# Performance work log

Measured on AMD Instinct MI355X. Metric: run time of the kernel, lower is better.

The kernel has to match this reference:

```python
import jax, jax.numpy as jnp
import numpy as np

DEPTH = 6
GAMMA = 1e-4
DIM = 1024
HIDDEN = 16
OUT_DIM = 64
N = 16384


def setup_inputs() -> dict:
    key = jax.random.key(0)
    k0, k1, k2, k3, k4 = jax.random.split(key, 5)
    X = jax.random.normal(k0, (N, DIM), dtype=jnp.float32)
    s1 = 1.0 / np.sqrt(DIM)
    s2 = 1.0 / np.sqrt(HIDDEN)
    W1 = jax.random.uniform(k1, (DIM, HIDDEN), jnp.float32, -s1, s1)
    b1 = jax.random.uniform(k2, (HIDDEN,), jnp.float32, -s1, s1)
    W2 = jax.random.uniform(k3, (HIDDEN, OUT_DIM), jnp.float32, -s2, s2)
    b2 = jax.random.uniform(k4, (OUT_DIM,), jnp.float32, -s2, s2)
    return {"X": X, "W1": W1, "b1": b1, "W2": W2, "b2": b2}


def _mlp(X, W1, b1, W2, b2):
    # shared FeedForwardClassifier: Linear(dim,16) -> ReLU -> Linear(16,out_dim)
    return jax.nn.relu(X @ W1 + b1) @ W2 + b2


def reference(X, W1, b1, W2, b2):
    for _ in range(DEPTH):
        # custom LayerNorm: row-wise L2 normalization (no eps in original)
        Xn = X / jnp.linalg.norm(X, axis=-1, keepdims=True)  # [N, dim]
        P = jax.nn.softmax(_mlp(Xn, W1, b1, W2, b2), axis=-1)  # [N, out_dim]
        # X + g*P@P.T@X - g*X@X.T@X, contracted small-Gram-first (same math)
        PtX = P.T @ Xn          # [out_dim, dim]
        G = Xn.T @ Xn           # [dim, dim]
        X = Xn + GAMMA * (P @ PtX) - GAMMA * (Xn @ G)
    return _mlp(X, W1, b1, W2, b2)
```

## Files before the change

kernel.cpp:

```cpp
#include <hip/hip_runtime.h>


#define N_ROWS 16384
#define DIM 1024
#define HID 16
#define OUTD 64
#define DEPTH 6
#define GAMMA 1e-4f

typedef short bf16x8 __attribute__((ext_vector_type(8)));
typedef unsigned short u16x8 __attribute__((ext_vector_type(8)));
typedef float f32x4 __attribute__((ext_vector_type(4)));

#define AS1C(p) ((const __attribute__((address_space(1))) void*)(p))
#define AS3(p)  ((__attribute__((address_space(3))) void*)(p))

__device__ __forceinline__ unsigned short f2bf(float f) {
    unsigned u = __builtin_bit_cast(unsigned, f);
    u += 0x7fffu + ((u >> 16) & 1u);
    return (unsigned short)(u >> 16);
}
__device__ __forceinline__ float b2f(ushort u) {
    unsigned x = ((unsigned)u) << 16;
    return __builtin_bit_cast(float, x);
}
__device__ __forceinline__ int swz(int n, int row) {
    return (n & ~63) | ((((n >> 3) & 7) ^ (row & 7)) << 3) | (n & 7);
}

__device__ __forceinline__ void atom_pk_bf16(ushort* p, ushort lo, ushort hi) {
#if __has_builtin(__builtin_amdgcn_global_atomic_fadd_v2bf16)
    typedef short s16x2 __attribute__((ext_vector_type(2)));
    s16x2 v;
    v[0] = (short)lo; v[1] = (short)hi;
    __builtin_amdgcn_global_atomic_fadd_v2bf16(
        (__attribute__((address_space(1))) s16x2*)p, v);
#else
    unsigned* up = (unsigned*)p;
    unsigned expected = *up;
    while (true) {
        float flo = b2f((ushort)(expected & 0xffffu)) + b2f(lo);
        float fhi = b2f((ushort)(expected >> 16)) + b2f(hi);
        unsigned desired = (unsigned)f2bf(flo) | ((unsigned)f2bf(fhi) << 16);
        unsigned old = atomicCAS(up, expected, desired);
        if (old == expected) break;
        expected = old;
    }
#endif
}

__global__ __launch_bounds__(256) void tobf16_k(const float* __restrict__ X,
        ushort* __restrict__ Xm, float* __restrict__ rinv) {
    int row = blockIdx.x, t = threadIdx.x;
    float4 v = ((const float4*)(X + (size_t)row * DIM))[t];
    ushort4 o4;
    o4.x = f2bf(v.x); o4.y = f2bf(v.y); o4.z = f2bf(v.z); o4.w = f2bf(v.w);
    *(ushort4*)(Xm + (size_t)row * DIM + swz(t * 4, row)) = o4;
    float ss = v.x * v.x + v.y * v.y + v.z * v.z + v.w * v.w;
    for (int o = 32; o > 0; o >>= 1) ss += __shfl_down(ss, o);
    __shared__ float wsum[4];
    if ((t & 63) == 0) wsum[t >> 6] = ss;
    __syncthreads();
    if (t == 0) rinv[row] = 1.0f / sqrtf(wsum[0] + wsum[1] + wsum[2] + wsum[3]);
}

__global__ __launch_bounds__(256) void rsqrt_k(const float* __restrict__ ssacc,
        float* __restrict__ rinv) {
    int i = blockIdx.x * 256 + threadIdx.x;
    rinv[i] = 1.0f / sqrtf(ssacc[i]);
}

__global__ __launch_bounds__(256) void transpose_k(const ushort* __restrict__ Xm,
        const float* __restrict__ rinv, ushort* __restrict__ XnT) {
    int r0 = blockIdx.x * 64;
    int c0 = blockIdx.y * 64;
    int t = threadIdx.x;
    __shared__ float ts[64 * 65];
    __shared__ float riS[64];
    if (t < 64) riS[t] = rinv[r0 + t];
    __syncthreads();
#pragma unroll
    for (int i = 0; i < 2; ++i) {
        int idx = i * 256 + t;
        int r = idx >> 3, lg = idx & 7;
        int rr = r0 + r;
        const ushort* p = Xm + (size_t)rr * DIM + c0 + ((lg ^ (rr & 7)) << 3);
        u16x8 a = *(const u16x8*)p;
        float s = riS[r];
        float* d = &ts[r * 65 + lg * 8];
#pragma unroll
        for (int u = 0; u < 8; ++u) d[u] = b2f(a[u]) * s;
    }
    __syncthreads();
#pragma unroll
    for (int i = 0; i < 2; ++i) {
        int g = i * 256 + t;
        int c = g >> 3;
        int rg = g & 7;
        u16x8 pk;
#pragma unroll
        for (int u = 0; u < 8; ++u) pk[u] = f2bf(ts[(rg * 8 + u) * 65 + c]);
        *(u16x8*)(XnT + (size_t)(c0 + c) * N_ROWS + r0 + ((rg ^ (c & 7)) << 3)) = pk;
    }
}

__global__ __launch_bounds__(256) void prep_w1t_k(const float* __restrict__ W1,
        ushort* __restrict__ W1T) {
    int idx = blockIdx.x * 256 + threadIdx.x;
    int h = idx >> 10, j = idx & 1023;
    W1T[idx] = f2bf(W1[j * HID + h]);
}

__global__ __launch_bounds__(256) void zgemm_k(const ushort* __restrict__ Xm,
        const ushort* __restrict__ W1T, const float* __restrict__ b1,
        float* __restrict__ z, const float* __restrict__ rv) {
    int t = threadIdx.x;
    int wave = t >> 6, lane = t & 63;
    int rl = lane & 15, q = lane >> 4;
    int rowbase = blockIdx.x * 64 + wave * 16;
    int m = rowbase + rl;
    int msw = m & 7;
    const ushort* arow = Xm + (size_t)m * DIM;
    const ushort* brow = W1T + (size_t)rl * DIM + q * 8;
    f32x4 acc = {0.f, 0.f, 0.f, 0.f};
#pragma unroll 8
    for (int kt = 0; kt < DIM; kt += 32) {
        int gl = ((kt >> 3) & 7) | q;
        int off = (kt & ~63) + ((gl ^ msw) << 3);
        bf16x8 a = *(const bf16x8*)(arow + off);
        bf16x8 b = *(const bf16x8*)(brow + kt);
        acc = __builtin_amdgcn_mfma_f32_16x16x32_bf16(a, b, acc, 0, 0, 0);
    }
#pragma unroll
    for (int rg = 0; rg < 4; ++rg) {
        int mm = rowbase + q * 4 + rg;
        float s = rv ? rv[mm] : 1.0f;
        z[(size_t)mm * HID + rl] = acc[rg] * s + b1[rl];
    }
}

__global__ __launch_bounds__(256) void head_k(const float* __restrict__ z,
        const float* __restrict__ W2, const float* __restrict__ b2,
        ushort* __restrict__ Pb, ushort* __restrict__ PTb,
        float* __restrict__ out, int do_softmax) {
    __shared__ float w2s[HID * OUTD];
    __shared__ float b2s[OUTD];
    int t = threadIdx.x;
    ((float4*)w2s)[t] = ((const float4*)W2)[t];
    if (t < OUTD) b2s[t] = b2[t];
    __syncthreads();
    int m = blockIdx.x * 256 + t;
    float h[HID];
    const float4* zp = (const float4*)(z + (size_t)m * HID);
#pragma unroll
    for (int i = 0; i < 4; ++i) {
        float4 v = zp[i];
        h[i * 4 + 0] = fmaxf(v.x, 0.f); h[i * 4 + 1] = fmaxf(v.y, 0.f);
        h[i * 4 + 2] = fmaxf(v.z, 0.f); h[i * 4 + 3] = fmaxf(v.w, 0.f);
    }
    float lo[OUTD];
#pragma unroll
    for (int o = 0; o < OUTD; ++o) lo[o] = b2s[o];
    for (int i = 0; i < HID; ++i) {
        float hv = h[i];
#pragma unroll
        for (int o = 0; o < OUTD; ++o) lo[o] += hv * w2s[i * OUTD + o];
    }
    if (do_softmax) {
        float mx = lo[0];
#pragma unroll
        for (int o = 1; o < OUTD; ++o) mx = fmaxf(mx, lo[o]);
        float sm = 0.f;
#pragma unroll
        for (int o = 0; o < OUTD; ++o) { float e = __expf(lo[o] - mx); lo[o] = e; sm += e; }
        float inv = 1.0f / sm;
#pragma unroll
        for (int o8 = 0; o8 < 8; ++o8) {
            u16x8 pk;
#pragma unroll
            for (int u = 0; u < 8; ++u) pk[u] = f2bf(lo[o8 * 8 + u] * inv);
            ((u16x8*)(Pb + (size_t)m * OUTD))[o8 ^ (m & 7)] = pk;
        }
#pragma unroll
        for (int o = 0; o < OUTD; ++o)
            PTb[(size_t)o * N_ROWS + swz(m, o)] = f2bf(lo[o] * inv);
    } else {
        float4* op = (float4*)(out + (size_t)m * OUTD);
#pragma unroll
        for (int o4 = 0; o4 < 16; ++o4) {
            float4 v; v.x = lo[o4 * 4 + 0]; v.y = lo[o4 * 4 + 1];
            v.z = lo[o4 * 4 + 2]; v.w = lo[o4 * 4 + 3];
            op[o4] = v;
        }
    }
}

__global__ __launch_bounds__(256) void castgp_k(const ushort* __restrict__ Gacc,
        const ushort* __restrict__ PtXacc, ushort* __restrict__ Gb,
        ushort* __restrict__ PtXTb) {
    int idx = blockIdx.x * 256 + threadIdx.x;
    if (idx < 262144) {
        int n = idx >> 8;
        int so = (idx & 255) * 4;
        int k0 = (so & ~63) | ((((so >> 3) & 7) ^ (n & 7)) << 3) | (so & 7);
        ushort4 o;
        ushort v0 = (k0 + 0 > n) ? Gacc[(size_t)n * DIM + k0 + 0] : Gacc[(size_t)(k0 + 0) * DIM + n];
        ushort v1 = (k0 + 1 > n) ? Gacc[(size_t)n * DIM + k0 + 1] : Gacc[(size_t)(k0 + 1) * DIM + n];
        ushort v2 = (k0 + 2 > n) ? Gacc[(size_t)n * DIM + k0 + 2] : Gacc[(size_t)(k0 + 2) * DIM + n];
        ushort v3 = (k0 + 3 > n) ? Gacc[(size_t)n * DIM + k0 + 3] : Gacc[(size_t)(k0 + 3) * DIM + n];
        o.x = v0 ^ 0x8000u; o.y = v1 ^ 0x8000u;
        o.z = v2 ^ 0x8000u; o.w = v3 ^ 0x8000u;
        *(ushort4*)(Gb + (size_t)n * DIM + so) = o;
    } else {
        int vv = idx - 262144;
        int d = vv >> 4;
        int so = (vv & 15) * 4;
        int k0 = ((((so >> 3) & 7) ^ (d & 7)) << 3) | (so & 7);
        const ushort* src = PtXacc + (size_t)d * OUTD + k0;
        ushort4 o;
        o.x = src[0]; o.y = src[1]; o.z = src[2]; o.w = src[3];
        *(ushort4*)(PtXTb + (size_t)d * OUTD + so) = o;
    }
}

template<int BM, int BN, int EPI, int TRI>
__global__ __launch_bounds__(256, 3) void gemm_nt_k(
        const ushort* __restrict__ A0, int lda0,
        const ushort* __restrict__ B0, int ldb0, int k0len,
        const ushort* __restrict__ A1, int lda1,
        const ushort* __restrict__ B1, int ldb1, int k1len,
        float* __restrict__ C, int ldc,
        const float* __restrict__ rinv, float gamma,
        float* __restrict__ ssacc) {
    constexpr int WTN = BN / 2;
    constexpr int NF = WTN / 16;
    constexpr int NAW = BM / 64;
    constexpr int NBW = BN / 64;
    __shared__ ushort ls[(BM + BN) * 64];
    ushort* lsA = ls;
    ushort* lsB = ls + BM * 64;
    int t = threadIdx.x;
    int wave = t >> 6, lane = t & 63;
    int rl = lane & 15, q = lane >> 4;
    int wm = wave & 1, wn = wave >> 1;
    int m0, n0, zidx;
    if (TRI) {
        int bid = blockIdx.x;
        int rest = bid >> 3;
        int bx = rest % 36, tm = 0;
        int zhi = rest / 36;
        zidx = (bid & 7) | (zhi << 3);
        while (bx >= 8 - tm) { bx -= 8 - tm; ++tm; }
        m0 = tm * 128; n0 = (tm + bx) * 128;
    } else {
        m0 = blockIdx.x * BM; n0 = blockIdx.y * BN; zidx = blockIdx.z;
    }
    int lrow8 = lane >> 3, lgrp = lane & 7;
    bool isA = wave < NAW;
    bool active = wave < NAW + NBW;
    int wlocal = isA ? wave : wave - NAW;
    ushort* dstb = ls + (isA ? 0 : BM * 64) + wlocal * 4096;

    f32x4 acc[4][NF];
#pragma unroll
    for (int i = 0; i < 4; ++i)
#pragma unroll
        for (int j = 0; j < NF; ++j) acc[i][j] = f32x4{0.f, 0.f, 0.f, 0.f};
    float rvv[4][4];

    for (int seg = 0; seg < 2; ++seg) {
        int klen = seg ? k1len : k0len;
        if (klen > 0) {
            const ushort* OPA = seg ? A1 : A0;
            const ushort* OPB = seg ? B1 : B0;
            int ldaS = seg ? lda1 : lda0;
            int ldbS = seg ? ldb1 : ldb0;
            int kb = seg ? 0 : zidx * k0len;
            const ushort* srcb;
            size_t ldS;
            if (isA) {
                srcb = OPA + (size_t)(m0 + wlocal * 64 + lrow8) * ldaS + lgrp * 8;
                ldS = (size_t)ldaS;
            } else {
                srcb = OPB + (size_t)(n0 + wlocal * 64 + lrow8) * ldbS + lgrp * 8;
                ldS = (size_t)ldbS;
            }
            srcb += kb;
            for (int kt = 0; kt < klen; kt += 64) {
                if (active) {
#pragma unroll
                    for (int c = 0; c < 8; ++c)
                        __builtin_amdgcn_global_load_lds(AS1C(srcb + c * 8 * ldS),
                                                         AS3(dstb + c * 512), 16, 0, 0);
                    srcb += 64;
                }
                __syncthreads();
#pragma unroll
                for (int s = 0; s < 2; ++s) {
                    bf16x8 af[4], bfr[NF];
#pragma unroll
                    for (int i = 0; i < 4; ++i) {
                        int row = wm * 64 + i * 16 + rl;
                        int sg = ((s << 2) | q) ^ (row & 7);
                        af[i] = *(const bf16x8*)&lsA[row * 64 + sg * 8];
                    }
#pragma unroll
                    for (int j = 0; j < NF; ++j) {
                        int row = wn * WTN + j * 16 + rl;
                        int sg = ((s << 2) | q) ^ (row & 7);
                        bfr[j] = *(const bf16x8*)&lsB[row * 64 + sg * 8];
                    }
#pragma unroll
                    for (int i = 0; i < 4; ++i)
#pragma unroll
                        for (int j = 0; j < NF; ++j)
                            acc[i][j] = __builtin_amdgcn_mfma_f32_16x16x32_bf16(
                                af[i], bfr[j], acc[i][j], 0, 0, 0);
                }
                __syncthreads();
            }
        }
        if (EPI == 1 && seg == 0) {
#pragma unroll
            for (int i = 0; i < 4; ++i)
#pragma unroll
                for (int rg = 0; rg < 4; ++rg)
                    rvv[i][rg] = rinv[m0 + wm * 64 + i * 16 + q * 4 + rg];
#pragma unroll
            for (int i = 0; i < 4; ++i)
#pragma unroll
                for (int j = 0; j < NF; ++j)
#pragma unroll
                    for (int rg = 0; rg < 4; ++rg)
                        acc[i][j][rg] *= rvv[i][rg];
        }
    }

    if (EPI == 0) {
        ushort* Cb = (ushort*)C;
#pragma unroll
        for (int i = 0; i < 4; ++i)
#pragma unroll
            for (int j = 0; j < NF; ++j)
#pragma unroll
                for (int rg = 0; rg < 4; ++rg) {
                    int m = m0 + wm * 64 + i * 16 + q * 4 + rg;
                    int n = n0 + wn * WTN + j * 16 + rl;
                    float v = acc[i][j][rg];
                    float vp = __shfl_xor(v, 1);
                    if ((rl & 1) == 0)
                        atom_pk_bf16(&Cb[(size_t)m * ldc + n], f2bf(v), f2bf(vp));
                }
    } else {
#pragma unroll
        for (int i = 0; i < 4; ++i)
#pragma unroll
            for (int rg = 0; rg < 4; ++rg) {
                int m = m0 + wm * 64 + i * 16 + q * 4 + rg;
                float ssl = 0.f;
#pragma unroll
                for (int j = 0; j < NF; ++j) {
                    int n = n0 + wn * WTN + j * 16 + rl;
                    int so = swz(n, m);
                    float base = b2f(A0[(size_t)m * lda0 + so]);
                    float vf = base * rvv[i][rg] + gamma * acc[i][j][rg];
                    ((ushort*)C)[(size_t)m * ldc + so] = f2bf(vf);
                    ssl += vf * vf;
                }
                ssl += __shfl_xor(ssl, 1);
                ssl += __shfl_xor(ssl, 2);
                ssl += __shfl_xor(ssl, 4);
                ssl += __shfl_xor(ssl, 8);
                if (rl == 0) atomicAdd(&ssacc[m], ssl);
            }
    }
}

extern "C" void kernel_launch(void* const* d_in, const int* in_sizes, int n_in,
                              void* d_out, int out_size, void* d_ws, size_t ws_size,
                              hipStream_t stream) {
    const float* X = (const float*)d_in[0];
    const float* W1 = (const float*)d_in[1];
    const float* b1 = (const float*)d_in[2];
    const float* W2 = (const float*)d_in[3];
    const float* b2 = (const float*)d_in[4];
    float* out = (float*)d_out;
    char* ws = (char*)d_ws;

    constexpr size_t O_BufA  = 0;
    constexpr size_t O_BufB  = O_BufA + (size_t)N_ROWS * DIM * 2;
    constexpr size_t O_Pb    = O_BufB + (size_t)N_ROWS * DIM * 2;
    constexpr size_t O_PTb   = O_Pb + (size_t)N_ROWS * OUTD * 2;
    constexpr size_t O_Gacc  = O_PTb + (size_t)OUTD * N_ROWS * 2;
    constexpr size_t O_PXacc = O_Gacc + (size_t)DIM * DIM * 2;
    constexpr size_t O_ssacc = O_PXacc + (size_t)DIM * OUTD * 2;
    constexpr size_t O_Gb    = O_ssacc + (size_t)N_ROWS * 4;
    constexpr size_t O_PtXTb = O_Gb + (size_t)DIM * DIM * 2;
    constexpr size_t O_riv   = O_PtXTb + (size_t)DIM * OUTD * 2;
    constexpr size_t O_z     = O_riv + (size_t)N_ROWS * 4;
    constexpr size_t O_W1T   = O_z + (size_t)N_ROWS * HID * 4;

    ushort* bufA  = (ushort*)(ws + O_BufA);
    ushort* bufB  = (ushort*)(ws + O_BufB);
    ushort* Pb    = (ushort*)(ws + O_Pb);
    ushort* PTb   = (ushort*)(ws + O_PTb);
    ushort* Gacc  = (ushort*)(ws + O_Gacc);
    ushort* PXacc = (ushort*)(ws + O_PXacc);
    float*  ssacc = (float*)(ws + O_ssacc);
    ushort* Gb    = (ushort*)(ws + O_Gb);
    ushort* PtXTb = (ushort*)(ws + O_PtXTb);
    float*  riv   = (float*)(ws + O_riv);
    float*  z     = (float*)(ws + O_z);
    ushort* W1T   = (ushort*)(ws + O_W1T);
    (void)in_sizes; (void)n_in; (void)out_size; (void)ws_size;

    prep_w1t_k<<<64, 256, 0, stream>>>(W1, W1T);
    tobf16_k<<<N_ROWS, 256, 0, stream>>>(X, bufA, riv);

    ushort* xm  = bufA;
    ushort* alt = bufB;

    for (int it = 0; it < DEPTH; ++it) {
        transpose_k<<<dim3(N_ROWS / 64, DIM / 64), 256, 0, stream>>>(xm, riv, alt);
        zgemm_k<<<N_ROWS / 64, 256, 0, stream>>>(xm, W1T, b1, z, riv);
        head_k<<<N_ROWS / 256, 256, 0, stream>>>(z, W2, b2, Pb, PTb, nullptr, 1);
        hipMemsetAsync(ws + O_Gacc, 0,
                       (size_t)DIM * DIM * 2 + (size_t)DIM * OUTD * 2
                       + (size_t)N_ROWS * 4, stream);
        gemm_nt_k<128, 128, 0, 1><<<dim3(8 * 36 * 2, 1, 1), 256, 0, stream>>>(
            alt, N_ROWS, alt, N_ROWS, 1024,
            nullptr, 0, nullptr, 0, 0,
            (float*)Gacc, DIM, nullptr, 0.f, nullptr);
        gemm_nt_k<128, 64, 0, 0><<<dim3(8, 1, 64), 256, 0, stream>>>(
            alt, N_ROWS, PTb, N_ROWS, 256,
            nullptr, 0, nullptr, 0, 0,
            (float*)PXacc, OUTD, nullptr, 0.f, nullptr);
        castgp_k<<<1088, 256, 0, stream>>>(Gacc, PXacc, Gb, PtXTb);
        gemm_nt_k<128, 128, 1, 0><<<dim3(N_ROWS / 128, DIM / 128, 1), 256, 0, stream>>>(
            xm, DIM, Gb, DIM, 1024,
            Pb, OUTD, PtXTb, OUTD, OUTD,
            (float*)alt, DIM, riv, GAMMA, ssacc);
        rsqrt_k<<<N_ROWS / 256, 256, 0, stream>>>(ssacc, riv);
        ushort* tmp = xm; xm = alt; alt = tmp;
    }

    zgemm_k<<<N_ROWS / 64, 256, 0, stream>>>(xm, W1T, b1, z, nullptr);
    head_k<<<N_ROWS / 256, 256, 0, stream>>>(z, W2, b2, Pb, PTb, out, 0);
}
```

Measured before the change: 1.100 ms.

## Replace bf16 atomic split-K accumulation with partial buffers reduced in cast kernel

```diff
diff --git a/kernel.cpp b/kernel.cpp
--- a/kernel.cpp
+++ b/kernel.cpp
@@ -26,27 +26,6 @@
 }
 __device__ __forceinline__ int swz(int n, int row) {
     return (n & ~63) | ((((n >> 3) & 7) ^ (row & 7)) << 3) | (n & 7);
-}
-
-__device__ __forceinline__ void atom_pk_bf16(ushort* p, ushort lo, ushort hi) {
-#if __has_builtin(__builtin_amdgcn_global_atomic_fadd_v2bf16)
-    typedef short s16x2 __attribute__((ext_vector_type(2)));
-    s16x2 v;
-    v[0] = (short)lo; v[1] = (short)hi;
-    __builtin_amdgcn_global_atomic_fadd_v2bf16(
-        (__attribute__((address_space(1))) s16x2*)p, v);
-#else
-    unsigned* up = (unsigned*)p;
-    unsigned expected = *up;
-    while (true) {
-        float flo = b2f((ushort)(expected & 0xffffu)) + b2f(lo);
-        float fhi = b2f((ushort)(expected >> 16)) + b2f(hi);
-        unsigned desired = (unsigned)f2bf(flo) | ((unsigned)f2bf(fhi) << 16);
-        unsigned old = atomicCAS(up, expected, desired);
-        if (old == expected) break;
-        expected = old;
-    }
-#endif
 }
 
 __global__ __launch_bounds__(256) void tobf16_k(const float* __restrict__ X,
@@ -195,30 +174,44 @@
     }
 }
 
-__global__ __launch_bounds__(256) void castgp_k(const ushort* __restrict__ Gacc,
-        const ushort* __restrict__ PtXacc, ushort* __restrict__ Gb,
+__global__ __launch_bounds__(256) void castgp_k(const ushort* __restrict__ Gp,
+        const ushort* __restrict__ PXp, ushort* __restrict__ Gb,
         ushort* __restrict__ PtXTb) {
     int idx = blockIdx.x * 256 + threadIdx.x;
     if (idx < 262144) {
         int n = idx >> 8;
         int so = (idx & 255) * 4;
         int k0 = (so & ~63) | ((((so >> 3) & 7) ^ (n & 7)) << 3) | (so & 7);
-        ushort4 o;
-        ushort v0 = (k0 + 0 > n) ? Gacc[(size_t)n * DIM + k0 + 0] : Gacc[(size_t)(k0 + 0) * DIM + n];
-        ushort v1 = (k0 + 1 > n) ? Gacc[(size_t)n * DIM + k0 + 1] : Gacc[(size_t)(k0 + 1) * DIM + n];
-        ushort v2 = (k0 + 2 > n) ? Gacc[(size_t)n * DIM + k0 + 2] : Gacc[(size_t)(k0 + 2) * DIM + n];
-        ushort v3 = (k0 + 3 > n) ? Gacc[(size_t)n * DIM + k0 + 3] : Gacc[(size_t)(k0 + 3) * DIM + n];
-        o.x = v0 ^ 0x8000u; o.y = v1 ^ 0x8000u;
-        o.z = v2 ^ 0x8000u; o.w = v3 ^ 0x8000u;
+        ushort po[4];
+#pragma unroll
+        for (int u = 0; u < 4; ++u) {
+            int kk = k0 + u;
+            int a = min(n, kk), b = max(n, kk);
+            int tm = a >> 7, tn = b >> 7;
+            int tlin = tm * 8 - ((tm * (tm - 1)) >> 1) + (tn - tm);
+            size_t off = (size_t)tlin * 16384 + (size_t)(a & 127) * 128 + (b & 127);
+            float v = 0.f;
+#pragma unroll
+            for (int zz = 0; zz < 4; ++zz) v += b2f(Gp[(size_t)zz * 589824 + off]);
+            po[u] = (ushort)(f2bf(v) ^ 0x8000u);
+        }
+        ushort4 o; o.x = po[0]; o.y = po[1]; o.z = po[2]; o.w = po[3];
         *(ushort4*)(Gb + (size_t)n * DIM + so) = o;
     } else {
         int vv = idx - 262144;
         int d = vv >> 4;
         int so = (vv & 15) * 4;
         int k0 = ((((so >> 3) & 7) ^ (d & 7)) << 3) | (so & 7);
-        const ushort* src = PtXacc + (size_t)d * OUTD + k0;
-        ushort4 o;
-        o.x = src[0]; o.y = src[1]; o.z = src[2]; o.w = src[3];
+        ushort po[4];
+#pragma unroll
+        for (int u = 0; u < 4; ++u) {
+            float v = 0.f;
+#pragma unroll
+            for (int zz = 0; zz < 8; ++zz)
+                v += b2f(PXp[(size_t)zz * 65536 + (size_t)d * OUTD + k0 + u]);
+            po[u] = f2bf(v);
+        }
+        ushort4 o; o.x = po[0]; o.y = po[1]; o.z = po[2]; o.w = po[3];
         *(ushort4*)(PtXTb + (size_t)d * OUTD + so) = o;
     }
 }
@@ -231,7 +224,7 @@
         const ushort* __restrict__ B1, int ldb1, int k1len,
         float* __restrict__ C, int ldc,
         const float* __restrict__ rinv, float gamma,
-        float* __restrict__ ssacc) {
+        float* __restrict__ ssacc, int pstride) {
     constexpr int WTN = BN / 2;
     constexpr int NF = WTN / 16;
     constexpr int NAW = BM / 64;
@@ -243,13 +236,12 @@
     int wave = t >> 6, lane = t & 63;
     int rl = lane & 15, q = lane >> 4;
     int wm = wave & 1, wn = wave >> 1;
-    int m0, n0, zidx;
+    int m0, n0, zidx, tlin = 0;
     if (TRI) {
         int bid = blockIdx.x;
-        int rest = bid >> 3;
-        int bx = rest % 36, tm = 0;
-        int zhi = rest / 36;
-        zidx = (bid & 7) | (zhi << 3);
+        zidx = bid & 3;
+        tlin = bid >> 2;
+        int bx = tlin, tm = 0;
         while (bx >= 8 - tm) { bx -= 8 - tm; ++tm; }
         m0 = tm * 128; n0 = (tm + bx) * 128;
     } else {
@@ -337,19 +329,26 @@
     }
 
     if (EPI == 0) {
-        ushort* Cb = (ushort*)C;
+        ushort* Cb = (ushort*)C + (size_t)zidx * (size_t)pstride;
 #pragma unroll
         for (int i = 0; i < 4; ++i)
 #pragma unroll
             for (int j = 0; j < NF; ++j)
 #pragma unroll
                 for (int rg = 0; rg < 4; ++rg) {
-                    int m = m0 + wm * 64 + i * 16 + q * 4 + rg;
-                    int n = n0 + wn * WTN + j * 16 + rl;
                     float v = acc[i][j][rg];
                     float vp = __shfl_xor(v, 1);
-                    if ((rl & 1) == 0)
-                        atom_pk_bf16(&Cb[(size_t)m * ldc + n], f2bf(v), f2bf(vp));
+                    if ((rl & 1) == 0) {
+                        int ml = wm * 64 + i * 16 + q * 4 + rg;
+                        int nl = wn * WTN + j * 16 + rl;
+                        size_t off;
+                        if (TRI)
+                            off = (size_t)tlin * (BM * BN) + (size_t)ml * BN + nl;
+                        else
+                            off = (size_t)(m0 + ml) * ldc + (n0 + nl);
+                        unsigned pk = (unsigned)f2bf(v) | ((unsigned)f2bf(vp) << 16);
+                        *(unsigned*)(Cb + off) = pk;
+                    }
                 }
     } else {
 #pragma unroll
@@ -387,31 +386,29 @@
     float* out = (float*)d_out;
     char* ws = (char*)d_ws;
 
-    constexpr size_t O_BufA  = 0;
-    constexpr size_t O_BufB  = O_BufA + (size_t)N_ROWS * DIM * 2;
-    constexpr size_t O_Pb    = O_BufB + (size_t)N_ROWS * DIM * 2;
-    constexpr size_t O_PTb   = O_Pb + (size_t)N_ROWS * OUTD * 2;
-    constexpr size_t O_Gacc  = O_PTb + (size_t)OUTD * N_ROWS * 2;
-    constexpr size_t O_PXacc = O_Gacc + (size_t)DIM * DIM * 2;
-    constexpr size_t O_ssacc = O_PXacc + (size_t)DIM * OUTD * 2;
-    constexpr size_t O_Gb    = O_ssacc + (size_t)N_ROWS * 4;
-    constexpr size_t O_PtXTb = O_Gb + (size_t)DIM * DIM * 2;
-    constexpr size_t O_riv   = O_PtXTb + (size_t)DIM * OUTD * 2;
-    constexpr size_t O_z     = O_riv + (size_t)N_ROWS * 4;
-    constexpr size_t O_W1T   = O_z + (size_t)N_ROWS * HID * 4;
+    constexpr size_t O_BufA    = 0;
+    constexpr size_t O_BufB    = O_BufA + (size_t)N_ROWS * DIM * 2;
+    constexpr size_t O_Pb      = O_BufB + (size_t)N_ROWS * DIM * 2;
+    constexpr size_t O_PTb     = O_Pb + (size_t)N_ROWS * OUTD * 2;
+    constexpr size_t O_Gb      = O_PTb + (size_t)OUTD * N_ROWS * 2;
+    constexpr size_t O_PtXTb   = O_Gb + (size_t)DIM * DIM * 2;
+    constexpr size_t O_riv     = O_PtXTb + (size_t)DIM * OUTD * 2;
+    constexpr size_t O_W1T     = O_riv + (size_t)N_ROWS * 4;
+    constexpr size_t O_ssacc   = O_W1T + (size_t)HID * DIM * 2;
+    constexpr size_t O_scratch = O_ssacc + (size_t)N_ROWS * 4;
 
     ushort* bufA  = (ushort*)(ws + O_BufA);
     ushort* bufB  = (ushort*)(ws + O_BufB);
     ushort* Pb    = (ushort*)(ws + O_Pb);
     ushort* PTb   = (ushort*)(ws + O_PTb);
-    ushort* Gacc  = (ushort*)(ws + O_Gacc);
-    ushort* PXacc = (ushort*)(ws + O_PXacc);
-    float*  ssacc = (float*)(ws + O_ssacc);
     ushort* Gb    = (ushort*)(ws + O_Gb);
     ushort* PtXTb = (ushort*)(ws + O_PtXTb);
     float*  riv   = (float*)(ws + O_riv);
-    float*  z     = (float*)(ws + O_z);
     ushort* W1T   = (ushort*)(ws + O_W1T);
+    float*  ssacc = (float*)(ws + O_ssacc);
+    float*  z     = (float*)(ws + O_scratch);
+    ushort* Gpart = (ushort*)(ws + O_scratch);
+    ushort* PXpart = (ushort*)d_out;
     (void)in_sizes; (void)n_in; (void)out_size; (void)ws_size;
 
     prep_w1t_k<<<64, 256, 0, stream>>>(W1, W1T);
@@ -424,22 +421,20 @@
         transpose_k<<<dim3(N_ROWS / 64, DIM / 64), 256, 0, stream>>>(xm, riv, alt);
         zgemm_k<<<N_ROWS / 64, 256, 0, stream>>>(xm, W1T, b1, z, riv);
         head_k<<<N_ROWS / 256, 256, 0, stream>>>(z, W2, b2, Pb, PTb, nullptr, 1);
-        hipMemsetAsync(ws + O_Gacc, 0,
-                       (size_t)DIM * DIM * 2 + (size_t)DIM * OUTD * 2
-                       + (size_t)N_ROWS * 4, stream);
-        gemm_nt_k<128, 128, 0, 1><<<dim3(8 * 36 * 2, 1, 1), 256, 0, stream>>>(
-            alt, N_ROWS, alt, N_ROWS, 1024,
+        gemm_nt_k<128, 128, 0, 1><<<dim3(36 * 4, 1, 1), 256, 0, stream>>>(
+            alt, N_ROWS, alt, N_ROWS, 4096,
             nullptr, 0, nullptr, 0, 0,
-            (float*)Gacc, DIM, nullptr, 0.f, nullptr);
-        gemm_nt_k<128, 64, 0, 0><<<dim3(8, 1, 64), 256, 0, stream>>>(
-            alt, N_ROWS, PTb, N_ROWS, 256,
+            (float*)Gpart, 128, nullptr, 0.f, nullptr, 36 * 16384);
+        gemm_nt_k<128, 64, 0, 0><<<dim3(8, 1, 8), 256, 0, stream>>>(
+            alt, N_ROWS, PTb, N_ROWS, 2048,
             nullptr, 0, nullptr, 0, 0,
-            (float*)PXacc, OUTD, nullptr, 0.f, nullptr);
-        castgp_k<<<1088, 256, 0, stream>>>(Gacc, PXacc, Gb, PtXTb);
+            (float*)PXpart, OUTD, nullptr, 0.f, nullptr, DIM * OUTD);
+        castgp_k<<<1088, 256, 0, stream>>>(Gpart, PXpart, Gb, PtXTb);
+        hipMemsetAsync(ws + O_ssacc, 0, (size_t)N_ROWS * 4, stream);
         gemm_nt_k<128, 128, 1, 0><<<dim3(N_ROWS / 128, DIM / 128, 1), 256, 0, stream>>>(
             xm, DIM, Gb, DIM, 1024,
             Pb, OUTD, PtXTb, OUTD, OUTD,
-            (float*)alt, DIM, riv, GAMMA, ssacc);
+            (float*)alt, DIM, riv, GAMMA, ssacc, 0);
         rsqrt_k<<<N_ROWS / 256, 256, 0, stream>>>(ssacc, riv);
         ushort* tmp = xm; xm = alt; alt = tmp;
     }
```

After: 1.200 ms. +9.1%, slower.
